# Kernel tuning notes

Hardware: AMD Instinct MI355X
Metric: run time of the kernel (lower is better)

Reference implementation:

```python
import jax, jax.numpy as jnp
import numpy as np

B, N, E = 4, 8192, 131072
NODE_F, EDGE_F, HID, ACT = 16, 1, 128, 8


def _glorot(key, shape):
    fan_in, fan_out = shape[0], shape[1]
    lim = np.sqrt(6.0 / (fan_in + fan_out))
    return jax.random.uniform(key, shape, jnp.float32, -lim, lim)


def setup_inputs() -> dict:
    key = jax.random.key(0)
    ks = jax.random.split(key, 20)
    inp = {
        'node_features': jax.random.randint(ks[0], (B, N, NODE_F), 0, 10, jnp.int32),
        'edge_index': jax.random.randint(ks[1], (B, 2, E), 0, N, jnp.int64),
        'edge_features': jax.random.normal(ks[2], (B, E, EDGE_F), jnp.float32),
        # conv1: in = 2*NODE_F + EDGE_F
        'c1_w1': _glorot(ks[3], (2 * NODE_F + EDGE_F, HID)), 'c1_b1': jnp.zeros((HID,), jnp.float32),
        'c1_w2': _glorot(ks[4], (HID, HID)), 'c1_b2': jnp.zeros((HID,), jnp.float32),
        # conv2/conv3: in = 2*HID + 1
        'c2_w1': _glorot(ks[5], (2 * HID + 1, HID)), 'c2_b1': jnp.zeros((HID,), jnp.float32),
        'c2_w2': _glorot(ks[6], (HID, HID)), 'c2_b2': jnp.zeros((HID,), jnp.float32),
        'c3_w1': _glorot(ks[7], (2 * HID + 1, HID)), 'c3_b1': jnp.zeros((HID,), jnp.float32),
        'c3_w2': _glorot(ks[8], (HID, HID)), 'c3_b2': jnp.zeros((HID,), jnp.float32),
        'lin_w': _glorot(ks[9], (NODE_F + HID, ACT)), 'lin_b': jnp.zeros((ACT,), jnp.float32),
    }
    return inp


def _edge_conv(x, src, dst, ea, w1, b1, w2, b2):
    # message: cat([x_i (target), x_j (source), edge_attr]) -> Linear -> LeakyReLU -> Linear
    m = jnp.concatenate([x[dst], x[src], ea], axis=1)          # [E, 2F+EF]
    m = jax.nn.leaky_relu(m @ w1 + b1) @ w2 + b2               # [E, out]
    out = jax.ops.segment_min(m, dst, num_segments=x.shape[0])  # min-aggregate at targets
    cnt = jnp.zeros((x.shape[0],), m.dtype).at[dst].add(1.0)
    return jnp.where(cnt[:, None] > 0, out, 0.0)                # nodes w/o in-edges -> 0 (PyG)


def _graph_fwd(x0, ei, ea, p):
    x0 = x0.astype(jnp.float32)  # torch casts to IntTensor then MLP promotes; math on integer values
    src, dst = ei[0], ei[1]      # flow='source_to_target'
    x = jax.nn.leaky_relu(_edge_conv(x0, src, dst, ea, p['c1_w1'], p['c1_b1'], p['c1_w2'], p['c1_b2']))
    x = jax.nn.leaky_relu(_edge_conv(x, src, dst, ea, p['c2_w1'], p['c2_b1'], p['c2_w2'], p['c2_b2']))
    x = jax.nn.leaky_relu(_edge_conv(x, src, dst, ea, p['c3_w1'], p['c3_b1'], p['c3_w2'], p['c3_b2']))
    x = jnp.concatenate([x0, x], axis=1)
    return jax.nn.softplus(x @ p['lin_w'] + p['lin_b'])         # [N, ACT]


def reference(node_features, edge_index, edge_features,
              c1_w1, c1_b1, c1_w2, c1_b2,
              c2_w1, c2_b1, c2_w2, c2_b2,
              c3_w1, c3_b1, c3_w2, c3_b2,
              lin_w, lin_b):
    p = dict(c1_w1=c1_w1, c1_b1=c1_b1, c1_w2=c1_w2, c1_b2=c1_b2,
             c2_w1=c2_w1, c2_b1=c2_b1, c2_w2=c2_w2, c2_b2=c2_b2,
             c3_w1=c3_w1, c3_b1=c3_b1, c3_w2=c3_w2, c3_b2=c3_b2,
             lin_w=lin_w, lin_b=lin_b)
    return jax.vmap(lambda x, ei, ea: _graph_fwd(x, ei, ea, p))(
        node_features, edge_index, edge_features)               # [B, N, ACT]
```

## Files before the change

### kernel.cpp

```cpp
#include <hip/hip_runtime.h>

#define B_ 4
#define N_ 8192
#define E_ 131072
#define HID_ 128

typedef unsigned short us8 __attribute__((ext_vector_type(8)));
typedef unsigned short us4 __attribute__((ext_vector_type(4)));
typedef unsigned int   ui4 __attribute__((ext_vector_type(4)));
typedef int            i4  __attribute__((ext_vector_type(4)));
typedef __bf16         v8bf __attribute__((ext_vector_type(8)));
typedef _Float16       hf8 __attribute__((ext_vector_type(8)));
typedef float          v4f  __attribute__((ext_vector_type(4)));
typedef float          v2f  __attribute__((ext_vector_type(2)));

#define KEY_INF 0xFF800000u

__device__ __forceinline__ float b2f(unsigned short u) {
    return __uint_as_float(((unsigned)u) << 16);
}
__device__ __forceinline__ unsigned short f2b(float f) {
    unsigned x = __float_as_uint(f);
    return (unsigned short)((x + 0x7fffu + ((x >> 16) & 1u)) >> 16);
}
__device__ __forceinline__ unsigned short f2h(float f) {
    union { _Float16 h; unsigned short u; } c; c.h = (_Float16)f; return c.u;
}
__device__ __forceinline__ unsigned fkey(float f) {
    unsigned b = __float_as_uint(f);
    return (b & 0x80000000u) ? ~b : (b | 0x80000000u);
}
__device__ __forceinline__ float funkey(unsigned k) {
    unsigned b = (k & 0x80000000u) ? (k ^ 0x80000000u) : ~k;
    return __uint_as_float(b);
}

__device__ __forceinline__ void repack_one(const float* __restrict__ w1, const float* __restrict__ w2,
                                           unsigned short* __restrict__ w1n, unsigned short* __restrict__ w2t,
                                           int F, int KPAD, int gid) {
    int t1 = 256 * KPAD;
    if (gid < t1) {
        int j = gid / KPAD, k = gid - j * KPAD;
        float v = 0.f;
        if (k < F) v = (j < 128) ? w1[k * 128 + j] : w1[(F + k) * 128 + (j - 128)];
        w1n[gid] = f2b(v);
    } else {
        int g = gid - t1;
        if (g < 16384) { int j = g >> 7, k = g & 127; w2t[g] = f2h(w2[k * 128 + j]); }
    }
}

__global__ void k_setup(const int* __restrict__ nf, unsigned short* __restrict__ x0b,
                        unsigned* __restrict__ cnt, unsigned* __restrict__ agg,
                        const float* __restrict__ w1a, const float* __restrict__ w2a,
                        const float* __restrict__ w1b, const float* __restrict__ w2b,
                        const float* __restrict__ w1c, const float* __restrict__ w2c,
                        unsigned short* __restrict__ w1n0, unsigned short* __restrict__ w2t0,
                        unsigned short* __restrict__ w1n1, unsigned short* __restrict__ w2t1,
                        unsigned short* __restrict__ w1n2, unsigned short* __restrict__ w2t2) {
    const int bid = blockIdx.x, tid = threadIdx.x;
    if (bid >= 4096) {
        const int rb = bid - 4096;
        const int gid = rb * 256 + tid;
        if (rb < 96)       repack_one(w1a, w2a, w1n0, w2t0, 16, 32, gid);
        else if (rb < 288) repack_one(w1b, w2b, w1n1, w2t1, 128, 128, gid - 96 * 256);
        else               repack_one(w1c, w2c, w1n2, w2t2, 128, 128, gid - 288 * 256);
        return;
    }
    const int gid = bid * 256 + tid;
    ui4 v = {KEY_INF, KEY_INF, KEY_INF, KEY_INF};
    ((ui4*)agg)[gid] = v;
    if (bid < 512) {
        i4 x = ((const i4*)nf)[gid];
        us4 o;
        o[0] = f2b((float)x[0]); o[1] = f2b((float)x[1]);
        o[2] = f2b((float)x[2]); o[3] = f2b((float)x[3]);
        ((us4*)x0b)[gid] = o;
    }
    if (bid < 128) cnt[gid] = 0u;
}

__global__ void k_hist(const int* __restrict__ ei, unsigned* __restrict__ cnt) {
    int gid = blockIdx.x * 256 + threadIdx.x;
    int b = gid >> 17, e = gid & (E_ - 1);
    int dst = ei[(b << 18) + E_ + e];
    atomicAdd(&cnt[(b << 13) + dst], 1u);
}

__global__ __launch_bounds__(1024) void k_scan(unsigned* __restrict__ cnt) {
    int b = blockIdx.x;
    __shared__ unsigned ps[1024];
    unsigned* c = cnt + (b << 13) + threadIdx.x * 8;
    unsigned loc[8]; unsigned s = 0;
#pragma unroll
    for (int i = 0; i < 8; i++) { loc[i] = c[i]; s += loc[i]; }
    ps[threadIdx.x] = s;
    __syncthreads();
    for (int off = 1; off < 1024; off <<= 1) {
        unsigned v = (threadIdx.x >= (unsigned)off) ? ps[threadIdx.x - off] : 0u;
        __syncthreads();
        ps[threadIdx.x] += v;
        __syncthreads();
    }
    unsigned run = ps[threadIdx.x] - s;
#pragma unroll
    for (int i = 0; i < 8; i++) { c[i] = run; run += loc[i]; }
}

template<int KPAD, bool FROM_AGG>
__device__ __forceinline__ void node_body(
    int bid,
    const unsigned short* __restrict__ xin,
    unsigned* __restrict__ agg,
    const unsigned short* __restrict__ w1n,
    const float* __restrict__ bias1,
    unsigned short* __restrict__ Yd,
    unsigned short* __restrict__ Ys,
    char* smem)
{
    constexpr int ASTR = KPAD + 8;
    unsigned short* A  = (unsigned short*)smem;
    unsigned short* Yb = (unsigned short*)(smem + 64 * ASTR * 2);

    const int tid = threadIdx.x;
    const int wave = tid >> 6, lane = tid & 63, lq = lane >> 4, lm = lane & 15;
    const int tile = (bid & 7) * 64 + (bid >> 3);
    const int n0 = tile * 64;

    v8bf wf[4][KPAD / 32]; float b1v[4];
#pragma unroll
    for (int nt = 0; nt < 4; nt++) {
        const int col = wave * 64 + nt * 16 + lm;
#pragma unroll
        for (int ks = 0; ks < KPAD / 32; ks++)
            wf[nt][ks] = *(const v8bf*)&w1n[col * KPAD + ks * 32 + lq * 8];
        b1v[nt] = (col < 128) ? bias1[col] : 0.f;
    }

    {
        const int row = tid >> 2, p = tid & 3;
        if (FROM_AGG) {
#pragma unroll
            for (int i = 0; i < 8; i++) {
                const int c = p + 4 * i;
                unsigned* ap = agg + ((size_t)(n0 + row)) * 128 + c * 4;
                ui4 k = *(ui4*)ap;
                ui4 inf = {KEY_INF, KEY_INF, KEY_INF, KEY_INF};
                *(ui4*)ap = inf;
                us4 o;
#pragma unroll
                for (int j = 0; j < 4; j++) {
                    float v = (k[j] == KEY_INF) ? 0.f : funkey(k[j]);
                    v = (v > 0.f) ? v : 0.01f * v;
                    o[j] = f2b(v);
                }
                *(us4*)&A[row * ASTR + c * 4] = o;
            }
        } else {
            us4 v = *(const us4*)(xin + ((size_t)(n0 + row)) * 16 + p * 4);
            *(us4*)&A[row * ASTR + p * 4] = v;
            us4 z = {0, 0, 0, 0};
            *(us4*)&A[row * ASTR + 16 + p * 4] = z;
        }
    }
    __syncthreads();

#pragma unroll
    for (int mt = 0; mt < 4; mt++) {
        v4f acc[4];
#pragma unroll
        for (int nt = 0; nt < 4; nt++) acc[nt] = v4f{0.f, 0.f, 0.f, 0.f};
#pragma unroll
        for (int ks = 0; ks < KPAD / 32; ks++) {
            v8bf a = *(const v8bf*)&A[(mt * 16 + lm) * ASTR + ks * 32 + lq * 8];
#pragma unroll
            for (int nt = 0; nt < 4; nt++)
                acc[nt] = __builtin_amdgcn_mfma_f32_16x16x32_bf16(a, wf[nt][ks], acc[nt], 0, 0, 0);
        }
#pragma unroll
        for (int nt = 0; nt < 4; nt++) {
            const int col = wave * 64 + nt * 16 + lm;
#pragma unroll
            for (int r = 0; r < 4; r++)
                Yb[(mt * 16 + lq * 4 + r) * 264 + col] = f2h(acc[nt][r] + b1v[nt]);
        }
    }
    __syncthreads();

    const int bb = tile >> 7, nl0 = (tile & 127) * 64;
#pragma unroll
    for (int i = 0; i < 8; i++) {
        const int idx = tid + 256 * i;
        const int row = idx >> 5, c = idx & 31;
        us8 v = *(const us8*)&Yb[row * 264 + c * 8];
        const int col0 = c * 8;
        unsigned short* dp = (col0 < 128)
            ? (Yd + ((size_t)(bb * N_) + nl0 + row) * 128 + col0)
            : (Ys + ((size_t)(bb * N_) + nl0 + row) * 128 + (col0 - 128));
        *(us8*)dp = v;
    }
}

template<int KPAD>
__global__ __launch_bounds__(256, 3) void k_node(
    const unsigned short* __restrict__ xin, unsigned* __restrict__ agg,
    const unsigned short* __restrict__ w1n, const float* __restrict__ bias1,
    unsigned short* __restrict__ Yd, unsigned short* __restrict__ Ys)
{
    __shared__ __align__(16) char smem[64 * (KPAD + 8) * 2 + 64 * 264 * 2];
    node_body<KPAD, true>(blockIdx.x, xin, agg, w1n, bias1, Yd, Ys, smem);
}

__global__ __launch_bounds__(256, 3) void k_scat_node1(
    const int* __restrict__ ei, unsigned* __restrict__ wptr, int* __restrict__ perm,
    const unsigned short* __restrict__ x0b,
    const unsigned short* __restrict__ w1n, const float* __restrict__ bias1,
    unsigned short* __restrict__ Yd, unsigned short* __restrict__ Ys)
{
    __shared__ __align__(16) char smem[64 * 40 * 2 + 64 * 264 * 2];
    const int bid = blockIdx.x;
    if (bid < 2048) {
        int gid = bid * 256 + threadIdx.x;
        int b = gid >> 17, e = gid & (E_ - 1);
        int dst = ei[(b << 18) + E_ + e];
        unsigned pos = atomicAdd(&wptr[(b << 13) + dst], 1u);
        perm[(b << 17) + pos] = e;
        return;
    }
    node_body<32, false>(bid - 2048, x0b, (unsigned*)nullptr, w1n, bias1, Yd, Ys, smem);
}

__global__ __launch_bounds__(256, 4) void k_edge(
    const unsigned short* __restrict__ Yd,
    const unsigned short* __restrict__ Ys,
    const int* __restrict__ ei,
    const float* __restrict__ eaf,
    const int* __restrict__ perm,
    const unsigned short* __restrict__ w2t,
    const float* __restrict__ weap,
    const float* __restrict__ bias2,
    unsigned* __restrict__ agg)
{
    __shared__ __align__(16) unsigned short Hs[2][64 * 128];
    __shared__ __align__(16) int      dstl[2][64];
    __shared__ __align__(16) _Float16 weal[128];

    const int tid = threadIdx.x;
    const int wave = tid >> 6, lane = tid & 63, lq = lane >> 4, lm = lane & 15;

    if (tid < 128) weal[tid] = (_Float16)weap[tid];

    hf8 w2f[2][4]; float b2v[2];
#pragma unroll
    for (int nt = 0; nt < 2; nt++) {
        const int col = wave * 32 + nt * 16 + lm;
#pragma unroll
        for (int ks = 0; ks < 4; ks++)
            w2f[nt][ks] = *(const hf8*)&w2t[col * 128 + ks * 32 + lq * 8];
        b2v[nt] = bias2[col];
    }
    __syncthreads();

    const int chunk = (blockIdx.x & 7) * 128 + (blockIdx.x >> 3);
    const int b = chunk >> 8;
    const int ebase = (b << 17) + (chunk & 255) * 512;

    const int arow = tid >> 2, p = tid & 3;
    const int lqg = (arow >> 2) & 3, mtg = arow >> 4, rg = arow & 3;
    const int sl  = lqg * 16 + mtg * 4 + rg;
    const int se0 = lqg * 128 + mtg * 4 + rg;
    const int rsw = arow & 15;

    const hf8 c01v = {(_Float16)0.01f, (_Float16)0.01f, (_Float16)0.01f, (_Float16)0.01f,
                      (_Float16)0.01f, (_Float16)0.01f, (_Float16)0.01f, (_Float16)0.01f};

    int e   = perm[ebase + se0];
    int src = ei[(b << 18) + e];
    int dst = ei[(b << 18) + E_ + e];
    float ea = eaf[(b << 17) + e];

    {
        const hf8* ydp = (const hf8*)(Yd + ((size_t)(b * N_) + dst) * 128);
        const hf8* ysp = (const hf8*)(Ys + ((size_t)(b * N_) + src) * 128);
        if (p == 0) dstl[0][sl] = dst;
        const _Float16 eh = (_Float16)ea;
        const hf8 ea8 = {eh, eh, eh, eh, eh, eh, eh, eh};
        hf8 va = ydp[p], vb = ysp[p];
#pragma unroll
        for (int i = 0; i < 4; i++) {
            hf8 na, nb;
            if (i < 3) { na = ydp[p + 4 * (i + 1)]; nb = ysp[p + 4 * (i + 1)]; }
            const int c = p + 4 * i;
            hf8 wv = *(const hf8*)&weal[c * 8];
            hf8 z = va + vb + wv * ea8;
            z = __builtin_elementwise_max(z, z * c01v);
            *(hf8*)&Hs[0][arow * 128 + ((c ^ rsw) * 8)] = z;
            va = na; vb = nb;
        }
    }
    __syncthreads();

    const int col0 = wave * 32 + lm, col1 = col0 + 16;
    unsigned* aggb = agg + (size_t)(b * N_) * 128;
    float cur0 = 0.f, cur1 = 0.f; int curd = -1; bool fseg = true;

    for (int jj = 0; jj < 8; jj++) {
        const int buf = jj & 1;

        if (jj < 7) {
            e   = perm[ebase + se0 + (jj + 1) * 16];
            src = ei[(b << 18) + e];
            dst = ei[(b << 18) + E_ + e];
            ea  = eaf[(b << 17) + e];
        }

        {
#pragma unroll
            for (int mt = 0; mt < 4; mt++) {
                const int row = mt * 16 + lm;
                v4f acc0 = {b2v[0], b2v[0], b2v[0], b2v[0]};
                v4f acc1 = {b2v[1], b2v[1], b2v[1], b2v[1]};
#pragma unroll
                for (int ks = 0; ks < 4; ks++) {
                    hf8 a = *(const hf8*)&Hs[buf][row * 128 + (((ks * 4 + lq) ^ lm) * 8)];
                    acc0 = __builtin_amdgcn_mfma_f32_16x16x32_f16(a, w2f[0][ks], acc0, 0, 0, 0);
                    acc1 = __builtin_amdgcn_mfma_f32_16x16x32_f16(a, w2f[1][ks], acc1, 0, 0, 0);
                }
                i4 dv = *(const i4*)&dstl[buf][lq * 16 + mt * 4];
#pragma unroll
                for (int r = 0; r < 4; r++) {
                    const float v0 = acc0[r];
                    const float v1 = acc1[r];
                    const int d = dv[r];
                    if (d != curd) {
                        if (curd >= 0) {
                            unsigned* p0 = aggb + (size_t)curd * 128 + col0;
                            unsigned* p1 = aggb + (size_t)curd * 128 + col1;
                            if (fseg) {
                                atomicMin(p0, fkey(cur0));
                                atomicMin(p1, fkey(cur1));
                            } else {
                                *p0 = fkey(cur0);
                                *p1 = fkey(cur1);
                            }
                            fseg = false;
                        }
                        curd = d; cur0 = v0; cur1 = v1;
                    } else {
                        cur0 = fminf(cur0, v0); cur1 = fminf(cur1, v1);
                    }
                }
            }
        }

        if (jj < 7) {
            const hf8* ydp = (const hf8*)(Yd + ((size_t)(b * N_) + dst) * 128);
            const hf8* ysp = (const hf8*)(Ys + ((size_t)(b * N_) + src) * 128);
            if (p == 0) dstl[buf ^ 1][sl] = dst;
            const _Float16 eh = (_Float16)ea;
            const hf8 ea8 = {eh, eh, eh, eh, eh, eh, eh, eh};
            hf8 va = ydp[p], vb = ysp[p];
#pragma unroll
            for (int i = 0; i < 4; i++) {
                hf8 na, nb;
                if (i < 3) { na = ydp[p + 4 * (i + 1)]; nb = ysp[p + 4 * (i + 1)]; }
                const int c = p + 4 * i;
                hf8 wv = *(const hf8*)&weal[c * 8];
                hf8 z = va + vb + wv * ea8;
                z = __builtin_elementwise_max(z, z * c01v);
                *(hf8*)&Hs[buf ^ 1][arow * 128 + ((c ^ rsw) * 8)] = z;
                va = na; vb = nb;
            }
        }
        __syncthreads();
    }

    atomicMin(aggb + (size_t)curd * 128 + col0, fkey(cur0));
    atomicMin(aggb + (size_t)curd * 128 + col1, fkey(cur1));
}

__global__ __launch_bounds__(256, 4) void k_final(
    const unsigned short* __restrict__ x0b, const unsigned* __restrict__ agg,
    const float* __restrict__ lw, const float* __restrict__ lb,
    float* __restrict__ out) {
    __shared__ float w[144 * 8];
    __shared__ float bias8[8];
    __shared__ float xs[64 * 129];
    const int tid = threadIdx.x;
    for (int i = tid; i < 1152; i += 256) w[i] = lw[i];
    if (tid < 8) bias8[tid] = lb[tid];
    const int n0 = blockIdx.x * 64;
#pragma unroll
    for (int i = 0; i < 8; i++) {
        const int idx = tid + 256 * i;
        const int row = idx >> 5, c = idx & 31;
        ui4 k = ((const ui4*)(agg + ((size_t)(n0 + row)) * 128))[c];
#pragma unroll
        for (int j = 0; j < 4; j++) {
            float v = (k[j] == KEY_INF) ? 0.f : funkey(k[j]);
            v = fmaxf(v, 0.01f * v);
            xs[row * 129 + c * 4 + j] = v;
        }
    }
    __syncthreads();
    const int node = tid >> 2, ap = (tid & 3) * 2;
    float a0 = bias8[ap], a1 = bias8[ap + 1];
    const unsigned short* x0 = x0b + (size_t)(n0 + node) * 16;
#pragma unroll
    for (int f = 0; f < 16; f++) {
        const float xv = b2f(x0[f]);
        a0 += xv * w[f * 8 + ap]; a1 += xv * w[f * 8 + ap + 1];
    }
    const float* xr = &xs[node * 129];
#pragma unroll 8
    for (int f = 0; f < 128; f++) {
        const float xv = xr[f];
        a0 += xv * w[(16 + f) * 8 + ap]; a1 += xv * w[(16 + f) * 8 + ap + 1];
    }
    v2f o;
    o[0] = fmaxf(a0, 0.f) + log1pf(expf(-fabsf(a0)));
    o[1] = fmaxf(a1, 0.f) + log1pf(expf(-fabsf(a1)));
    *(v2f*)&out[(size_t)(n0 + node) * 8 + ap] = o;
}

extern "C" void kernel_launch(void* const* d_in, const int* in_sizes, int n_in,
                              void* d_out, int out_size, void* d_ws, size_t ws_size,
                              hipStream_t stream) {
    (void)in_sizes; (void)n_in; (void)out_size; (void)ws_size;
    const int* nf  = (const int*)d_in[0];
    const int* ei  = (const int*)d_in[1];
    const float* eaf = (const float*)d_in[2];
    const float* cw1[3] = {(const float*)d_in[3],  (const float*)d_in[7],  (const float*)d_in[11]};
    const float* cb1[3] = {(const float*)d_in[4],  (const float*)d_in[8],  (const float*)d_in[12]};
    const float* cw2[3] = {(const float*)d_in[5],  (const float*)d_in[9],  (const float*)d_in[13]};
    const float* cb2[3] = {(const float*)d_in[6],  (const float*)d_in[10], (const float*)d_in[14]};
    const float* lw = (const float*)d_in[15];
    const float* lb = (const float*)d_in[16];
    float* out = (float*)d_out;

    size_t off = 0;
    auto carve = [&](size_t bytes) { void* p = (char*)d_ws + off; off += (bytes + 255) & ~(size_t)255; return p; };
    unsigned short* x0b  = (unsigned short*)carve((size_t)B_ * N_ * 16 * 2);
    unsigned*       agg  = (unsigned*)carve((size_t)B_ * N_ * 128 * 4);
    unsigned*       cnt  = (unsigned*)carve((size_t)B_ * N_ * 4);
    int*            perm = (int*)carve((size_t)B_ * E_ * 4);
    unsigned short* Yd   = (unsigned short*)carve((size_t)B_ * N_ * 128 * 2);
    unsigned short* Ys   = (unsigned short*)carve((size_t)B_ * N_ * 128 * 2);
    unsigned short* w1n0 = (unsigned short*)carve(256 * 32 * 2);
    unsigned short* w2t0 = (unsigned short*)carve(128 * 128 * 2);
    unsigned short* w1n1 = (unsigned short*)carve(256 * 128 * 2);
    unsigned short* w2t1 = (unsigned short*)carve(128 * 128 * 2);
    unsigned short* w1n2 = (unsigned short*)carve(256 * 128 * 2);
    unsigned short* w2t2 = (unsigned short*)carve(128 * 128 * 2);

    k_setup<<<4576, 256, 0, stream>>>(nf, x0b, cnt, agg,
                                      cw1[0], cw2[0], cw1[1], cw2[1], cw1[2], cw2[2],
                                      w1n0, w2t0, w1n1, w2t1, w1n2, w2t2);
    k_hist<<<2048, 256, 0, stream>>>(ei, cnt);
    k_scan<<<B_, 1024, 0, stream>>>(cnt);

    k_scat_node1<<<2560, 256, 0, stream>>>(ei, cnt, perm, x0b, w1n0, cb1[0], Yd, Ys);
    k_edge<<<1024, 256, 0, stream>>>(Yd, Ys, ei, eaf, perm, w2t0, cw1[0] + 32 * 128, cb2[0], agg);

    k_node<128><<<512, 256, 0, stream>>>(x0b, agg, w1n1, cb1[1], Yd, Ys);
    k_edge<<<1024, 256, 0, stream>>>(Yd, Ys, ei, eaf, perm, w2t1, cw1[1] + 256 * 128, cb2[1], agg);

    k_node<128><<<512, 256, 0, stream>>>(x0b, agg, w1n2, cb1[2], Yd, Ys);
    k_edge<<<1024, 256, 0, stream>>>(Yd, Ys, ei, eaf, perm, w2t2, cw1[2] + 256 * 128, cb2[2], agg);

    k_final<<<512, 256, 0, stream>>>(x0b, agg, lw, lb, out);
}
```

Measured before the change: 290.5 us.

## Software-pipeline edge index and row gathers one stage deeper ahead of MFMA

Restructures the edge-conv loop so the edge permutation and indices are fetched two iterations ahead. The gathered Yd/Ys rows for the next tile are issued before the MFMA and min-aggregation work on the current tile, rather than after it. This lets the dependent global-memory chain (perm → ei → row gather) overlap with compute. The cost is more live registers (eight hf8 row values plus the extra index variables), which could raise register pressure and reduce occupancy.

```diff
diff --git a/kernel.cpp b/kernel.cpp
--- a/kernel.cpp
+++ b/kernel.cpp
@@ -274,44 +274,70 @@
     const hf8 c01v = {(_Float16)0.01f, (_Float16)0.01f, (_Float16)0.01f, (_Float16)0.01f,
                       (_Float16)0.01f, (_Float16)0.01f, (_Float16)0.01f, (_Float16)0.01f};
 
-    int e   = perm[ebase + se0];
-    int src = ei[(b << 18) + e];
-    int dst = ei[(b << 18) + E_ + e];
-    float ea = eaf[(b << 17) + e];
-
+    const int eib = b << 18, eab = b << 17;
+    const size_t nb = (size_t)(b * N_);
+
+    int eA   = perm[ebase + se0];
+    int srcA = ei[eib + eA];
+    int dstA = ei[eib + E_ + eA];
+    float eaA = eaf[eab + eA];
+
+    int eB = perm[ebase + se0 + 16];
+
+    hf8 ry0, ry1, ry2, ry3, rs0, rs1, rs2, rs3;
     {
-        const hf8* ydp = (const hf8*)(Yd + ((size_t)(b * N_) + dst) * 128);
-        const hf8* ysp = (const hf8*)(Ys + ((size_t)(b * N_) + src) * 128);
-        if (p == 0) dstl[0][sl] = dst;
-        const _Float16 eh = (_Float16)ea;
+        const hf8* ydp = (const hf8*)(Yd + (nb + dstA) * 128);
+        const hf8* ysp = (const hf8*)(Ys + (nb + srcA) * 128);
+        ry0 = ydp[p]; ry1 = ydp[p + 4]; ry2 = ydp[p + 8]; ry3 = ydp[p + 12];
+        rs0 = ysp[p]; rs1 = ysp[p + 4]; rs2 = ysp[p + 8]; rs3 = ysp[p + 12];
+        if (p == 0) dstl[0][sl] = dstA;
+    }
+    int srcB = ei[eib + eB];
+    int dstB = ei[eib + E_ + eB];
+    float eaB = eaf[eab + eB];
+
+    {
+        const _Float16 eh = (_Float16)eaA;
         const hf8 ea8 = {eh, eh, eh, eh, eh, eh, eh, eh};
-        hf8 va = ydp[p], vb = ysp[p];
-#pragma unroll
-        for (int i = 0; i < 4; i++) {
-            hf8 na, nb;
-            if (i < 3) { na = ydp[p + 4 * (i + 1)]; nb = ysp[p + 4 * (i + 1)]; }
-            const int c = p + 4 * i;
-            hf8 wv = *(const hf8*)&weal[c * 8];
-            hf8 z = va + vb + wv * ea8;
-            z = __builtin_elementwise_max(z, z * c01v);
-            *(hf8*)&Hs[0][arow * 128 + ((c ^ rsw) * 8)] = z;
-            va = na; vb = nb;
-        }
+        hf8 z;
+        z = ry0 + rs0 + (*(const hf8*)&weal[p * 8]) * ea8;
+        z = __builtin_elementwise_max(z, z * c01v);
+        *(hf8*)&Hs[0][arow * 128 + ((p ^ rsw) * 8)] = z;
+        z = ry1 + rs1 + (*(const hf8*)&weal[(p + 4) * 8]) * ea8;
+        z = __builtin_elementwise_max(z, z * c01v);
+        *(hf8*)&Hs[0][arow * 128 + (((p + 4) ^ rsw) * 8)] = z;
+        z = ry2 + rs2 + (*(const hf8*)&weal[(p + 8) * 8]) * ea8;
+        z = __builtin_elementwise_max(z, z * c01v);
+        *(hf8*)&Hs[0][arow * 128 + (((p + 8) ^ rsw) * 8)] = z;
+        z = ry3 + rs3 + (*(const hf8*)&weal[(p + 12) * 8]) * ea8;
+        z = __builtin_elementwise_max(z, z * c01v);
+        *(hf8*)&Hs[0][arow * 128 + (((p + 12) ^ rsw) * 8)] = z;
     }
     __syncthreads();
 
     const int col0 = wave * 32 + lm, col1 = col0 + 16;
-    unsigned* aggb = agg + (size_t)(b * N_) * 128;
+    unsigned* aggb = agg + nb * 128;
     float cur0 = 0.f, cur1 = 0.f; int curd = -1; bool fseg = true;
 
     for (int jj = 0; jj < 8; jj++) {
         const int buf = jj & 1;
 
+        int eC = 0;
+        if (jj < 6) eC = perm[ebase + se0 + (jj + 2) * 16];
+
         if (jj < 7) {
-            e   = perm[ebase + se0 + (jj + 1) * 16];
-            src = ei[(b << 18) + e];
-            dst = ei[(b << 18) + E_ + e];
-            ea  = eaf[(b << 17) + e];
+            const hf8* ydp = (const hf8*)(Yd + (nb + dstB) * 128);
+            const hf8* ysp = (const hf8*)(Ys + (nb + srcB) * 128);
+            ry0 = ydp[p]; ry1 = ydp[p + 4]; ry2 = ydp[p + 8]; ry3 = ydp[p + 12];
+            rs0 = ysp[p]; rs1 = ysp[p + 4]; rs2 = ysp[p + 8]; rs3 = ysp[p + 12];
+            if (p == 0) dstl[buf ^ 1][sl] = dstB;
+        }
+
+        int srcC = 0, dstC = 0; float eaC = 0.f;
+        if (jj < 6) {
+            srcC = ei[eib + eC];
+            dstC = ei[eib + E_ + eC];
+            eaC  = eaf[eab + eC];
         }
 
         {
@@ -354,23 +380,22 @@
         }
 
         if (jj < 7) {
-            const hf8* ydp = (const hf8*)(Yd + ((size_t)(b * N_) + dst) * 128);
-            const hf8* ysp = (const hf8*)(Ys + ((size_t)(b * N_) + src) * 128);
-            if (p == 0) dstl[buf ^ 1][sl] = dst;
-            const _Float16 eh = (_Float16)ea;
+            const _Float16 eh = (_Float16)eaB;
             const hf8 ea8 = {eh, eh, eh, eh, eh, eh, eh, eh};
-            hf8 va = ydp[p], vb = ysp[p];
-#pragma unroll
-            for (int i = 0; i < 4; i++) {
-                hf8 na, nb;
-                if (i < 3) { na = ydp[p + 4 * (i + 1)]; nb = ysp[p + 4 * (i + 1)]; }
-                const int c = p + 4 * i;
-                hf8 wv = *(const hf8*)&weal[c * 8];
-                hf8 z = va + vb + wv * ea8;
-                z = __builtin_elementwise_max(z, z * c01v);
-                *(hf8*)&Hs[buf ^ 1][arow * 128 + ((c ^ rsw) * 8)] = z;
-                va = na; vb = nb;
-            }
+            hf8 z;
+            z = ry0 + rs0 + (*(const hf8*)&weal[p * 8]) * ea8;
+            z = __builtin_elementwise_max(z, z * c01v);
+            *(hf8*)&Hs[buf ^ 1][arow * 128 + ((p ^ rsw) * 8)] = z;
+            z = ry1 + rs1 + (*(const hf8*)&weal[(p + 4) * 8]) * ea8;
+            z = __builtin_elementwise_max(z, z * c01v);
+            *(hf8*)&Hs[buf ^ 1][arow * 128 + (((p + 4) ^ rsw) * 8)] = z;
+            z = ry2 + rs2 + (*(const hf8*)&weal[(p + 8) * 8]) * ea8;
+            z = __builtin_elementwise_max(z, z * c01v);
+            *(hf8*)&Hs[buf ^ 1][arow * 128 + (((p + 8) ^ rsw) * 8)] = z;
+            z = ry3 + rs3 + (*(const hf8*)&weal[(p + 12) * 8]) * ea8;
+            z = __builtin_elementwise_max(z, z * c01v);
+            *(hf8*)&Hs[buf ^ 1][arow * 128 + (((p + 12) ^ rsw) * 8)] = z;
+            srcB = srcC; dstB = dstC; eaB = eaC;
         }
         __syncthreads();
     }
```

Result: slower. 311.6 us (+7.2%).

## Build MFMA A-operands directly in registers and stage W2 in LDS

Applied to the files above, without the earlier changes.

The edge kernel now gathers Yd/Ys rows straight into the register layout of the MFMA A operand and no longer writes the hidden tile through double-buffered shared memory. That removes the per-iteration __syncthreads. W2 moves from registers into swizzled LDS, and each wave now covers 64 output columns for its own half of the edges. Each wave streams 16 rows per step with software prefetch of indices and features. The cost is reading W2 from LDS on every MFMA, and each wave now gathers feature rows redundantly, since both column-half waves load the same edges.

```diff
diff --git a/kernel.cpp b/kernel.cpp
--- a/kernel.cpp
+++ b/kernel.cpp
@@ -241,142 +241,148 @@
     const float* __restrict__ bias2,
     unsigned* __restrict__ agg)
 {
-    __shared__ __align__(16) unsigned short Hs[2][64 * 128];
-    __shared__ __align__(16) int      dstl[2][64];
-    __shared__ __align__(16) _Float16 weal[128];
+    __shared__ __align__(16) unsigned short w2lds[128 * 128 / 8 * 8];
 
     const int tid = threadIdx.x;
     const int wave = tid >> 6, lane = tid & 63, lq = lane >> 4, lm = lane & 15;
 
-    if (tid < 128) weal[tid] = (_Float16)weap[tid];
-
-    hf8 w2f[2][4]; float b2v[2];
-#pragma unroll
-    for (int nt = 0; nt < 2; nt++) {
-        const int col = wave * 32 + nt * 16 + lm;
-#pragma unroll
-        for (int ks = 0; ks < 4; ks++)
-            w2f[nt][ks] = *(const hf8*)&w2t[col * 128 + ks * 32 + lq * 8];
-        b2v[nt] = bias2[col];
-    }
+    {
+        const int col = tid >> 1, cb = (tid & 1) * 8, key = col & 15;
+#pragma unroll
+        for (int u = 0; u < 8; u++) {
+            const int c = cb + u;
+            hf8 v = *(const hf8*)&w2t[col * 128 + c * 8];
+            *(hf8*)((char*)w2lds + col * 256 + ((c ^ key) * 16)) = v;
+        }
+    }
+
+    hf8 wl0, wl1, wl2, wl3;
+    {
+        const float* wp = weap + lq * 8;
+#pragma unroll
+        for (int u = 0; u < 8; u++) {
+            wl0[u] = (_Float16)wp[u];
+            wl1[u] = (_Float16)wp[32 + u];
+            wl2[u] = (_Float16)wp[64 + u];
+            wl3[u] = (_Float16)wp[96 + u];
+        }
+    }
+
+    const int cbase = (wave & 1) * 64;
+    const float b20 = bias2[cbase + lm],      b21 = bias2[cbase + 16 + lm];
+    const float b22 = bias2[cbase + 32 + lm], b23 = bias2[cbase + 48 + lm];
+
     __syncthreads();
+
+    const char* w2b  = (const char*)w2lds + (cbase + lm) * 256;
+    const char* w2p0 = w2b + ((( 0 + lq) ^ lm) * 16);
+    const char* w2p1 = w2b + ((( 4 + lq) ^ lm) * 16);
+    const char* w2p2 = w2b + ((( 8 + lq) ^ lm) * 16);
+    const char* w2p3 = w2b + (((12 + lq) ^ lm) * 16);
 
     const int chunk = (blockIdx.x & 7) * 128 + (blockIdx.x >> 3);
     const int b = chunk >> 8;
     const int ebase = (b << 17) + (chunk & 255) * 512;
-
-    const int arow = tid >> 2, p = tid & 3;
-    const int lqg = (arow >> 2) & 3, mtg = arow >> 4, rg = arow & 3;
-    const int sl  = lqg * 16 + mtg * 4 + rg;
-    const int se0 = lqg * 128 + mtg * 4 + rg;
-    const int rsw = arow & 15;
+    const int h = wave >> 1;
+    const int eib = b << 18, eab = b << 17;
+    const size_t nb = (size_t)(b * N_);
+
+    const int pA = ebase + h * 256 + ((lm >> 2) << 6) + (lm & 3);
 
     const hf8 c01v = {(_Float16)0.01f, (_Float16)0.01f, (_Float16)0.01f, (_Float16)0.01f,
                       (_Float16)0.01f, (_Float16)0.01f, (_Float16)0.01f, (_Float16)0.01f};
 
-    int e   = perm[ebase + se0];
-    int src = ei[(b << 18) + e];
-    int dst = ei[(b << 18) + E_ + e];
-    float ea = eaf[(b << 17) + e];
-
+    int pe = perm[pA];
+    int sA = ei[eib + pe], dA = ei[eib + E_ + pe];
+    float eA = eaf[eab + pe];
+
+    hf8 ry0, ry1, ry2, ry3, rs0, rs1, rs2, rs3;
     {
-        const hf8* ydp = (const hf8*)(Yd + ((size_t)(b * N_) + dst) * 128);
-        const hf8* ysp = (const hf8*)(Ys + ((size_t)(b * N_) + src) * 128);
-        if (p == 0) dstl[0][sl] = dst;
-        const _Float16 eh = (_Float16)ea;
+        const hf8* ydp = (const hf8*)(Yd + (nb + dA) * 128);
+        const hf8* ysp = (const hf8*)(Ys + (nb + sA) * 128);
+        ry0 = ydp[lq]; ry1 = ydp[4 + lq]; ry2 = ydp[8 + lq]; ry3 = ydp[12 + lq];
+        rs0 = ysp[lq]; rs1 = ysp[4 + lq]; rs2 = ysp[8 + lq]; rs3 = ysp[12 + lq];
+    }
+    pe = perm[pA + 4];
+    int sB = ei[eib + pe], dB = ei[eib + E_ + pe];
+    float eB = eaf[eab + pe];
+
+    unsigned* aggb = agg + nb * 128;
+    float cur0 = 0.f, cur1 = 0.f, cur2 = 0.f, cur3 = 0.f;
+    int curd = -1; bool fseg = true;
+
+    for (int jj = 0; jj < 16; jj++) {
+        if (jj < 14) pe = perm[pA + (jj + 2) * 4];
+
+        const _Float16 eh = (_Float16)eA;
         const hf8 ea8 = {eh, eh, eh, eh, eh, eh, eh, eh};
-        hf8 va = ydp[p], vb = ysp[p];
-#pragma unroll
-        for (int i = 0; i < 4; i++) {
-            hf8 na, nb;
-            if (i < 3) { na = ydp[p + 4 * (i + 1)]; nb = ysp[p + 4 * (i + 1)]; }
-            const int c = p + 4 * i;
-            hf8 wv = *(const hf8*)&weal[c * 8];
-            hf8 z = va + vb + wv * ea8;
-            z = __builtin_elementwise_max(z, z * c01v);
-            *(hf8*)&Hs[0][arow * 128 + ((c ^ rsw) * 8)] = z;
-            va = na; vb = nb;
-        }
-    }
-    __syncthreads();
-
-    const int col0 = wave * 32 + lm, col1 = col0 + 16;
-    unsigned* aggb = agg + (size_t)(b * N_) * 128;
-    float cur0 = 0.f, cur1 = 0.f; int curd = -1; bool fseg = true;
-
-    for (int jj = 0; jj < 8; jj++) {
-        const int buf = jj & 1;
-
-        if (jj < 7) {
-            e   = perm[ebase + se0 + (jj + 1) * 16];
-            src = ei[(b << 18) + e];
-            dst = ei[(b << 18) + E_ + e];
-            ea  = eaf[(b << 17) + e];
-        }
-
-        {
-#pragma unroll
-            for (int mt = 0; mt < 4; mt++) {
-                const int row = mt * 16 + lm;
-                v4f acc0 = {b2v[0], b2v[0], b2v[0], b2v[0]};
-                v4f acc1 = {b2v[1], b2v[1], b2v[1], b2v[1]};
-#pragma unroll
-                for (int ks = 0; ks < 4; ks++) {
-                    hf8 a = *(const hf8*)&Hs[buf][row * 128 + (((ks * 4 + lq) ^ lm) * 8)];
-                    acc0 = __builtin_amdgcn_mfma_f32_16x16x32_f16(a, w2f[0][ks], acc0, 0, 0, 0);
-                    acc1 = __builtin_amdgcn_mfma_f32_16x16x32_f16(a, w2f[1][ks], acc1, 0, 0, 0);
+        hf8 af0 = ry0 + rs0 + wl0 * ea8; af0 = __builtin_elementwise_max(af0, af0 * c01v);
+        hf8 af1 = ry1 + rs1 + wl1 * ea8; af1 = __builtin_elementwise_max(af1, af1 * c01v);
+        hf8 af2 = ry2 + rs2 + wl2 * ea8; af2 = __builtin_elementwise_max(af2, af2 * c01v);
+        hf8 af3 = ry3 + rs3 + wl3 * ea8; af3 = __builtin_elementwise_max(af3, af3 * c01v);
+
+        if (jj < 15) {
+            const hf8* ydp = (const hf8*)(Yd + (nb + dB) * 128);
+            const hf8* ysp = (const hf8*)(Ys + (nb + sB) * 128);
+            ry0 = ydp[lq]; ry1 = ydp[4 + lq]; ry2 = ydp[8 + lq]; ry3 = ydp[12 + lq];
+            rs0 = ysp[lq]; rs1 = ysp[4 + lq]; rs2 = ysp[8 + lq]; rs3 = ysp[12 + lq];
+        }
+
+        v4f a0 = {b20, b20, b20, b20};
+        v4f a1 = {b21, b21, b21, b21};
+        v4f a2 = {b22, b22, b22, b22};
+        v4f a3 = {b23, b23, b23, b23};
+#define MMROW(AF, WP) \
+        a0 = __builtin_amdgcn_mfma_f32_16x16x32_f16(AF, *(const hf8*)(WP),          a0, 0, 0, 0); \
+        a1 = __builtin_amdgcn_mfma_f32_16x16x32_f16(AF, *(const hf8*)((WP) + 4096), a1, 0, 0, 0); \
+        a2 = __builtin_amdgcn_mfma_f32_16x16x32_f16(AF, *(const hf8*)((WP) + 8192), a2, 0, 0, 0); \
+        a3 = __builtin_amdgcn_mfma_f32_16x16x32_f16(AF, *(const hf8*)((WP) + 12288), a3, 0, 0, 0);
+        MMROW(af0, w2p0)
+        MMROW(af1, w2p1)
+        MMROW(af2, w2p2)
+        MMROW(af3, w2p3)
+#undef MMROW
+
+#pragma unroll
+        for (int r = 0; r < 4; r++) {
+            const int d = __shfl(dA, lq * 4 + r);
+            if (d != curd) {
+                if (curd >= 0) {
+                    unsigned* pp = aggb + (size_t)curd * 128 + cbase + lm;
+                    if (fseg) {
+                        atomicMin(pp,      fkey(cur0));
+                        atomicMin(pp + 16, fkey(cur1));
+                        atomicMin(pp + 32, fkey(cur2));
+                        atomicMin(pp + 48, fkey(cur3));
+                    } else {
+                        pp[0]  = fkey(cur0);
+                        pp[16] = fkey(cur1);
+                        pp[32] = fkey(cur2);
+                        pp[48] = fkey(cur3);
+                    }
+                    fseg = false;
                 }
-                i4 dv = *(const i4*)&dstl[buf][lq * 16 + mt * 4];
-#pragma unroll
-                for (int r = 0; r < 4; r++) {
-                    const float v0 = acc0[r];
-                    const float v1 = acc1[r];
-                    const int d = dv[r];
-                    if (d != curd) {
-                        if (curd >= 0) {
-                            unsigned* p0 = aggb + (size_t)curd * 128 + col0;
-                            unsigned* p1 = aggb + (size_t)curd * 128 + col1;
-                            if (fseg) {
-                                atomicMin(p0, fkey(cur0));
-                                atomicMin(p1, fkey(cur1));
-                            } else {
-                                *p0 = fkey(cur0);
-                                *p1 = fkey(cur1);
-                            }
-                            fseg = false;
-                        }
-                        curd = d; cur0 = v0; cur1 = v1;
-                    } else {
-                        cur0 = fminf(cur0, v0); cur1 = fminf(cur1, v1);
-                    }
-                }
+                curd = d;
+                cur0 = a0[r]; cur1 = a1[r]; cur2 = a2[r]; cur3 = a3[r];
+            } else {
+                cur0 = fminf(cur0, a0[r]); cur1 = fminf(cur1, a1[r]);
+                cur2 = fminf(cur2, a2[r]); cur3 = fminf(cur3, a3[r]);
             }
         }
 
-        if (jj < 7) {
-            const hf8* ydp = (const hf8*)(Yd + ((size_t)(b * N_) + dst) * 128);
-            const hf8* ysp = (const hf8*)(Ys + ((size_t)(b * N_) + src) * 128);
-            if (p == 0) dstl[buf ^ 1][sl] = dst;
-            const _Float16 eh = (_Float16)ea;
-            const hf8 ea8 = {eh, eh, eh, eh, eh, eh, eh, eh};
-            hf8 va = ydp[p], vb = ysp[p];
-#pragma unroll
-            for (int i = 0; i < 4; i++) {
-                hf8 na, nb;
-                if (i < 3) { na = ydp[p + 4 * (i + 1)]; nb = ysp[p + 4 * (i + 1)]; }
-                const int c = p + 4 * i;
-                hf8 wv = *(const hf8*)&weal[c * 8];
-                hf8 z = va + vb + wv * ea8;
-                z = __builtin_elementwise_max(z, z * c01v);
-                *(hf8*)&Hs[buf ^ 1][arow * 128 + ((c ^ rsw) * 8)] = z;
-                va = na; vb = nb;
-            }
-        }
-        __syncthreads();
-    }
-
-    atomicMin(aggb + (size_t)curd * 128 + col0, fkey(cur0));
-    atomicMin(aggb + (size_t)curd * 128 + col1, fkey(cur1));
+        sA = sB; dA = dB; eA = eB;
+        if (jj < 14) {
+            sB = ei[eib + pe]; dB = ei[eib + E_ + pe]; eB = eaf[eab + pe];
+        }
+    }
+
+    {
+        unsigned* pp = aggb + (size_t)curd * 128 + cbase + lm;
+        atomicMin(pp,      fkey(cur0));
+        atomicMin(pp + 16, fkey(cur1));
+        atomicMin(pp + 32, fkey(cur2));
+        atomicMin(pp + 48, fkey(cur3));
+    }
 }
 
 __global__ __launch_bounds__(256, 4) void k_final(
```

Result: slower. 994.6 us (+242.3%).
